# Optimization experiments

Measured on AMD Instinct MI355X. Metric: run time of the kernel, lower is better.

Reference implementation:

```python
import jax, jax.numpy as jnp
import numpy as np

# Dimensions: state [N, d, n, 2] with last axis = (q, p)
N, D, NN = 256, 8, 32
FEAT = D * NN          # flattened q features = 256
HID = 256              # MLP hidden width
DT = 0.01              # integration step
STEPS = 100            # number of RK4 steps (sequential)


def setup_inputs() -> dict:
    key = jax.random.key(0)
    k0, k1, k2 = jax.random.split(key, 3)
    x0 = 0.1 * jax.random.normal(k0, (N, D, NN, 2), dtype=jnp.float32)
    W1 = jax.random.normal(k1, (FEAT, HID), dtype=jnp.float32) / np.float32(np.sqrt(FEAT))
    b1 = jnp.zeros((HID,), dtype=jnp.float32)
    W2 = jax.random.normal(k2, (HID, 1), dtype=jnp.float32) / np.float32(np.sqrt(HID))
    b2 = jnp.zeros((1,), dtype=jnp.float32)
    return {"x0": x0, "W1": W1, "b1": b1, "W2": W2, "b2": b2}


def _hamiltonian(x, W1, b1, W2, b2):
    # x: [N, d, n, 2] -> H: [N]
    q = x[..., 0]
    p = x[..., 1]
    kinetic = 0.5 * jnp.sum(p * p, axis=(1, 2))          # [N]
    qf = q.reshape(q.shape[0], -1)                        # [N, d*n]
    h = jnp.tanh(qf @ W1 + b1)                            # [N, HID]
    V = (h @ W2 + b2)[:, 0]                               # [N]
    return kinetic + V


def _vector_field(x, params):
    # Hamiltonian vector field: dq/dt = dH/dp, dp/dt = -dH/dq (t-independent)
    g = jax.grad(lambda xx: jnp.sum(_hamiltonian(xx, *params)))(x)  # [N,d,n,2]
    return jnp.stack([g[..., 1], -g[..., 0]], axis=-1)


def _rk4_step(x, eps, params):
    k1 = _vector_field(x, params)
    k2 = _vector_field(x + 0.5 * eps * k1, params)
    k3 = _vector_field(x + 0.5 * eps * k2, params)
    k4 = _vector_field(x + eps * k3, params)
    return x + (eps / 6.0) * (k1 + 2.0 * k2 + 2.0 * k3 + k4)


def reference(x0, W1, b1, W2, b2):
    params = (W1, b1, W2, b2)
    eps = jnp.float32(DT)

    def step(x, _):
        return _rk4_step(x, eps, params), None

    xT, _ = jax.lax.scan(step, x0, None, length=STEPS)
    return xT
```

## Files before the change

kernel.cpp:

```cpp
#include <hip/hip_runtime.h>
#include <stdint.h>


typedef _Float16 v8h __attribute__((ext_vector_type(8)));
typedef float v4f __attribute__((ext_vector_type(4)));

#define NSTEPS 100
#define NEX 25
#define US 272

#define MFMA_AV(C, A, B) \
    asm("v_mfma_f32_16x16x32_f16 %0, %1, %2, %0" : "+v"(C) : "v"(A), "a"(B))

__device__ __forceinline__ float bfly4(float x) {
    float a = x, b = x;
    asm("v_permlane16_swap_b32 %0, %1" : "+v"(a), "+v"(b));
    float s = a + b;
    float c = s, d = s;
    asm("v_permlane32_swap_b32 %0, %1" : "+v"(c), "+v"(d));
    return c + d;
}

__device__ __forceinline__ float ueval2(float zz, float w4) {
    float e_ = __expf(zz);
    float r_ = __builtin_amdgcn_rcpf(e_ + 1.f);
    return w4 * __builtin_fmaf(-r_, r_, r_);
}

__global__ __launch_bounds__(256)
void ham_setup(const float* __restrict__ W1, _Float16* __restrict__ wt,
               _Float16* __restrict__ mf)
{
    const int b = blockIdx.x;
    const int t = threadIdx.x;
    wt[b * 256 + t] = (_Float16)W1[t * 256 + b];
    float acc = 0.f;
    #pragma unroll 4
    for (int r = 0; r < 256; ++r) {
        float wk = (float)(_Float16)W1[r * 256 + b];
        float wc = (float)(_Float16)W1[r * 256 + t];
        acc = __builtin_fmaf(wk, wc, acc);
    }
    mf[b * 256 + t] = (_Float16)acc;
}

__global__ __launch_bounds__(1024, 4)
void ham_kernel(const float* __restrict__ x0, const float* __restrict__ W1,
                const float* __restrict__ b1, const float* __restrict__ W2,
                const _Float16* __restrict__ wt, const _Float16* __restrict__ mf,
                float* __restrict__ out)
{
    __shared__ __align__(128) _Float16 ubuf[2 * 16 * US];

    const int t = threadIdx.x;
    const int w = t >> 6;
    const int l = t & 63;
    const int quad = l >> 4;
    const int s = l & 15;
    const int c0 = 16 * w + s;
    const int blk = blockIdx.x;
    const int kq = 8 * quad;
    const int sel = (s & 3) * US;

    v8h wF0[8], wM0[8];
    #pragma unroll
    for (int kk = 0; kk < 8; ++kk) {
        wF0[kk] = *(const v8h*)(wt + c0 * 256 + 32 * kk + kq);
        wM0[kk] = *(const v8h*)(mf + c0 * 256 + 32 * kk + kq);
    }

    const float b1r0 = b1[c0];
    const float w4 = 4.f * W2[c0];
    float2 qp0 = ((const float2*)(x0 + (size_t)blk * 512))[c0];
    const float q0o0 = qp0.x, p0o0 = qp0.y;

    if (quad == 0) {
        ubuf[c0] = (_Float16)q0o0;
        ubuf[US + c0] = (_Float16)p0o0;
        ubuf[2 * US + c0] = (_Float16)0.f;
        ubuf[3 * US + c0] = (_Float16)0.f;
    }
    __syncthreads();
    float z1, P;
    {
        const _Float16* ab = ubuf + sel + 8 * quad;
        v4f C0a = {0.f,0.f,0.f,0.f}, C0b = {0.f,0.f,0.f,0.f};
        #pragma unroll
        for (int kk = 0; kk < 8; kk += 2) {
            v8h a0 = *(const v8h*)(ab + 32 * kk);
            v8h a1 = *(const v8h*)(ab + 32 * (kk + 1));
            C0a = __builtin_amdgcn_mfma_f32_16x16x32_f16(a0, wF0[kk], C0a, 0, 0, 0);
            C0b = __builtin_amdgcn_mfma_f32_16x16x32_f16(a1, wF0[kk + 1], C0b, 0, 0, 0);
        }
        v4f C0s = C0a + C0b;
        z1 = C0s[0] + b1r0;  P = C0s[1];
    }
    __syncthreads();

    const float dt = 0.01f, hdt = 0.005f, dt6 = 0.01f / 6.f;
    const float dtdt6 = dt * dt6, hdt2 = hdt * hdt, dthdt = dt * hdt;
    const float fourdt = 4.f * dt;
    const float qf  = (float)quad;
    const float cPn   = -(qf * 0.25f * dt6);
    const float K2cz1 = 2.f * qf * dt;
    const float K2B   = qf * (4.f - qf) * dtdt6 * 0.25f;
    const float K2Vn  = -(qf * dtdt6 * 0.5f);
    const float K2hdt = 2.f * hdt;
    const float K2hdt2n = -2.f * hdt2;
    const float K2dt  = 2.f * dt;
    const float K2dthdtn = -2.f * dthdt;
    const float wB  = 3.f - qf;

    const int cw = c0 ^ (quad << 3);
    const int R0 = 4 * quad;
    const int wo0 = (R0 + 0) * US + cw;
    const int wo1 = (R0 + 1) * US + (cw ^ 32);
    const int wo2 = (R0 + 2) * US + cw;
    const int wo3 = (R0 + 3) * US + (cw ^ 32);
    const int sx = (s >> 2) & 3;
    const int rbase = s * US + 8 * (quad ^ sx);
    const int sodd = (s & 1) << 5;
    const _Float16* pe = ubuf + rbase + sodd;
    const _Float16* po = ubuf + rbase + 32 - sodd;

    float SBp = 0.f, SVp = 0.f;
    float Y1L = 0.f, Y2L = 0.f;
    float S1p = 0.f, S23p = 0.f;
    float cn = 99.f - qf;

    #pragma unroll 1
    for (int e = 0; e < NEX; ++e) {
        const int bo = (e & 1) * (16 * US);

        float Pp  = __builtin_fmaf(cPn, SBp, P);
        float zp2 = __builtin_fmaf(K2cz1, P, z1 + z1);
        zp2 = __builtin_fmaf(K2B, SBp, zp2);
        zp2 = __builtin_fmaf(K2Vn, SVp, zp2);
        float zb2 = __builtin_fmaf(K2hdt, Pp, zp2);
        float zc2 = __builtin_fmaf(K2hdt2n, Y1L, zb2);
        float zd2 = __builtin_fmaf(K2dt, Pp, zp2);
        zd2 = __builtin_fmaf(K2dthdtn, Y2L, zd2);

        float ua = ueval2(zp2, w4);
        float ub = ueval2(zb2, w4);
        float uc = ueval2(zc2, w4);
        float ud = ueval2(zd2, w4);

        ubuf[bo + wo0] = (_Float16)ua;
        ubuf[bo + wo1] = (_Float16)ub;
        ubuf[bo + wo2] = (_Float16)uc;
        ubuf[bo + wo3] = (_Float16)ud;
        __syncthreads();

        v4f C0s;
        {
            v4f C0a = {0.f,0.f,0.f,0.f}, C0b = {0.f,0.f,0.f,0.f};
            #pragma unroll
            for (int kk = 0; kk < 8; kk += 2) {
                v8h a0 = *(const v8h*)(pe + bo + 32 * kk);
                v8h a1 = *(const v8h*)(po + bo + 32 * kk);
                MFMA_AV(C0a, a0, wM0[kk]);
                MFMA_AV(C0b, a1, wM0[kk + 1]);
            }
            C0s = C0a + C0b;
        }

        float Y1 = C0s[0], Y2 = C0s[1], Y3 = C0s[2], Y4 = C0s[3];
        float tA = Y2 + Y3;
        float A  = Y1 + tA;
        float B  = A + tA + Y4;
        float V  = __builtin_fmaf(wB, B, A);
        float SB = bfly4(B);
        float SV = bfly4(V);

        z1 = __builtin_fmaf(fourdt, P, z1);
        z1 = __builtin_fmaf(-dtdt6, SV, z1);
        P  = __builtin_fmaf(-dt6, SB, P);

        SBp = SB;  SVp = SV;  Y1L = Y1;  Y2L = Y2;

        float tv = ub + uc;
        float sp = __builtin_fmaf(2.f, tv, ua + ud);
        float sq = ua + tv;
        S1p += sp;
        S23p = __builtin_fmaf(cn, sp, S23p) + sq;
        cn -= 4.f;
    }

    v8h wBt0[8];
    #pragma unroll
    for (int kk = 0; kk < 8; ++kk) {
        const float* wp = W1 + c0 * 256 + 32 * kk + kq;
        v4f lo = *(const v4f*)(wp);
        v4f hi = *(const v4f*)(wp + 4);
        v8h h;
        h[0] = (_Float16)lo[0]; h[1] = (_Float16)lo[1];
        h[2] = (_Float16)lo[2]; h[3] = (_Float16)lo[3];
        h[4] = (_Float16)hi[0]; h[5] = (_Float16)hi[1];
        h[6] = (_Float16)hi[2]; h[7] = (_Float16)hi[3];
        wBt0[kk] = h;
    }

    const float S1f  = bfly4(S1p);
    const float S23f = bfly4(S23p);
    __syncthreads();
    if (quad == 0) {
        ubuf[c0] = (_Float16)S1f;
        ubuf[US + c0] = (_Float16)S23f;
        ubuf[2 * US + c0] = (_Float16)0.f;
        ubuf[3 * US + c0] = (_Float16)0.f;
    }
    __syncthreads();
    float D10, D20;
    {
        const _Float16* ab = ubuf + sel + 8 * quad;
        v4f C0a = {0.f,0.f,0.f,0.f}, C0b = {0.f,0.f,0.f,0.f};
        #pragma unroll
        for (int kk = 0; kk < 8; kk += 2) {
            v8h a0 = *(const v8h*)(ab + 32 * kk);
            v8h a1 = *(const v8h*)(ab + 32 * (kk + 1));
            C0a = __builtin_amdgcn_mfma_f32_16x16x32_f16(a0, wBt0[kk], C0a, 0, 0, 0);
            C0b = __builtin_amdgcn_mfma_f32_16x16x32_f16(a1, wBt0[kk + 1], C0b, 0, 0, 0);
        }
        v4f C0s = C0a + C0b;
        D10 = C0s[0];  D20 = C0s[1];
    }
    const float dt6e = 0.01f / 6.f, dtdt6e = 0.01f * dt6e;
    float pT0 = p0o0 - dt6e * D10;
    float qT0 = q0o0 + 0.01f * (float)NSTEPS * p0o0 - dtdt6e * D20;

    if (quad == 0)
        ((float2*)(out + (size_t)blk * 512))[c0] = make_float2(qT0, pT0);
}

extern "C" void kernel_launch(void* const* d_in, const int* in_sizes, int n_in,
                              void* d_out, int out_size, void* d_ws, size_t ws_size,
                              hipStream_t stream) {
    const float* x0 = (const float*)d_in[0];
    const float* W1 = (const float*)d_in[1];
    const float* b1 = (const float*)d_in[2];
    const float* W2 = (const float*)d_in[3];
    float* out = (float*)d_out;
    _Float16* wt = (_Float16*)d_ws;
    _Float16* mf = wt + 256 * 256;
    hipLaunchKernelGGL(ham_setup, dim3(256), dim3(256), 0, stream, W1, wt, mf);
    hipLaunchKernelGGL(ham_kernel, dim3(256), dim3(1024), 0, stream,
                       x0, W1, b1, W2, wt, mf, out);
}
```

Measured before the change: 109.9 us.

## Shrink block to 4 waves, each thread handling four hidden columns

The main kernel now launches 256 threads per block instead of 1024. Each thread owns four hidden units, holding four sets of weight fragments in registers and issuing four MFMA chains per step. The shared buffer layout moves from padded rows to an XOR swizzle with vectorized 4-wide half stores. Block barriers become cheaper, and the setup kernel reuses a shared column of W1 instead of reloading it. The cost is more serial MFMA and transcendental work per wave, plus higher register pressure, which could lengthen the sequential per-step critical path.

```diff
diff --git a/kernel.cpp b/kernel.cpp
--- a/kernel.cpp
+++ b/kernel.cpp
@@ -3,11 +3,10 @@
 
 
 typedef _Float16 v8h __attribute__((ext_vector_type(8)));
+typedef _Float16 v4h __attribute__((ext_vector_type(4)));
 typedef float v4f __attribute__((ext_vector_type(4)));
 
-#define NSTEPS 100
 #define NEX 25
-#define US 272
 
 #define MFMA_AV(C, A, B) \
     asm("v_mfma_f32_16x16x32_f16 %0, %1, %2, %0" : "+v"(C) : "v"(A), "a"(B))
@@ -31,69 +30,92 @@
 void ham_setup(const float* __restrict__ W1, _Float16* __restrict__ wt,
                _Float16* __restrict__ mf)
 {
+    __shared__ float colb[256];
     const int b = blockIdx.x;
     const int t = threadIdx.x;
-    wt[b * 256 + t] = (_Float16)W1[t * 256 + b];
+    float wv = W1[t * 256 + b];
+    wt[b * 256 + t] = (_Float16)wv;
+    colb[t] = (float)(_Float16)wv;
+    __syncthreads();
     float acc = 0.f;
-    #pragma unroll 4
+    #pragma unroll 8
     for (int r = 0; r < 256; ++r) {
-        float wk = (float)(_Float16)W1[r * 256 + b];
         float wc = (float)(_Float16)W1[r * 256 + t];
-        acc = __builtin_fmaf(wk, wc, acc);
+        acc = __builtin_fmaf(colb[r], wc, acc);
     }
     mf[b * 256 + t] = (_Float16)acc;
 }
 
-__global__ __launch_bounds__(1024, 4)
+__global__ __launch_bounds__(256, 1)
 void ham_kernel(const float* __restrict__ x0, const float* __restrict__ W1,
                 const float* __restrict__ b1, const float* __restrict__ W2,
                 const _Float16* __restrict__ wt, const _Float16* __restrict__ mf,
                 float* __restrict__ out)
 {
-    __shared__ __align__(128) _Float16 ubuf[2 * 16 * US];
+    __shared__ __align__(128) _Float16 ubuf[2 * 16 * 256];
 
     const int t = threadIdx.x;
     const int w = t >> 6;
     const int l = t & 63;
     const int quad = l >> 4;
     const int s = l & 15;
-    const int c0 = 16 * w + s;
     const int blk = blockIdx.x;
     const int kq = 8 * quad;
-    const int sel = (s & 3) * US;
-
-    v8h wF0[8], wM0[8];
+    const int cb = 64 * w + 4 * s;
+    const int chb = cb >> 3;
+    const int clo = cb & 7;
+
+    v8h wM[4][8];
     #pragma unroll
-    for (int kk = 0; kk < 8; ++kk) {
-        wF0[kk] = *(const v8h*)(wt + c0 * 256 + 32 * kk + kq);
-        wM0[kk] = *(const v8h*)(mf + c0 * 256 + 32 * kk + kq);
-    }
-
-    const float b1r0 = b1[c0];
-    const float w4 = 4.f * W2[c0];
-    float2 qp0 = ((const float2*)(x0 + (size_t)blk * 512))[c0];
-    const float q0o0 = qp0.x, p0o0 = qp0.y;
+    for (int tt = 0; tt < 4; ++tt)
+        #pragma unroll
+        for (int kk = 0; kk < 8; ++kk)
+            wM[tt][kk] = *(const v8h*)(mf + (cb + tt) * 256 + 32 * kk + kq);
+
+    float b1r[4], w4v[4];
+    #pragma unroll
+    for (int tt = 0; tt < 4; ++tt) {
+        b1r[tt] = b1[cb + tt];
+        w4v[tt] = 4.f * W2[cb + tt];
+    }
+    v4f qp01 = *(const v4f*)(x0 + (size_t)blk * 512 + 2 * cb);
+    v4f qp23 = *(const v4f*)(x0 + (size_t)blk * 512 + 2 * cb + 4);
+    float q0v[4] = {qp01[0], qp01[2], qp23[0], qp23[2]};
+    float p0v[4] = {qp01[1], qp01[3], qp23[1], qp23[3]};
 
     if (quad == 0) {
-        ubuf[c0] = (_Float16)q0o0;
-        ubuf[US + c0] = (_Float16)p0o0;
-        ubuf[2 * US + c0] = (_Float16)0.f;
-        ubuf[3 * US + c0] = (_Float16)0.f;
-    }
-    __syncthreads();
-    float z1, P;
+        v4h r0 = {(_Float16)q0v[0], (_Float16)q0v[1],
+                  (_Float16)q0v[2], (_Float16)q0v[3]};
+        v4h r1 = {(_Float16)p0v[0], (_Float16)p0v[1],
+                  (_Float16)p0v[2], (_Float16)p0v[3]};
+        v4h rz = {(_Float16)0.f, (_Float16)0.f, (_Float16)0.f, (_Float16)0.f};
+        *(v4h*)(ubuf + 0 * 256 + 8 * (chb ^ 0) + clo) = r0;
+        *(v4h*)(ubuf + 1 * 256 + 8 * (chb ^ 1) + clo) = r1;
+        *(v4h*)(ubuf + 2 * 256 + 8 * (chb ^ 2) + clo) = rz;
+        *(v4h*)(ubuf + 3 * 256 + 8 * (chb ^ 3) + clo) = rz;
+    }
+    __syncthreads();
+    float z1[4], P[4];
     {
-        const _Float16* ab = ubuf + sel + 8 * quad;
-        v4f C0a = {0.f,0.f,0.f,0.f}, C0b = {0.f,0.f,0.f,0.f};
-        #pragma unroll
-        for (int kk = 0; kk < 8; kk += 2) {
-            v8h a0 = *(const v8h*)(ab + 32 * kk);
-            v8h a1 = *(const v8h*)(ab + 32 * (kk + 1));
-            C0a = __builtin_amdgcn_mfma_f32_16x16x32_f16(a0, wF0[kk], C0a, 0, 0, 0);
-            C0b = __builtin_amdgcn_mfma_f32_16x16x32_f16(a1, wF0[kk + 1], C0b, 0, 0, 0);
-        }
-        v4f C0s = C0a + C0b;
-        z1 = C0s[0] + b1r0;  P = C0s[1];
+        const _Float16* ab = ubuf + (s & 3) * 256 + 8 * (quad ^ (s & 3));
+        v8h a[8];
+        #pragma unroll
+        for (int kk = 0; kk < 8; ++kk)
+            a[kk] = *(const v8h*)(ab + 32 * kk);
+        #pragma unroll
+        for (int tt = 0; tt < 4; ++tt) {
+            v4f Ca = {0.f,0.f,0.f,0.f}, Cb = {0.f,0.f,0.f,0.f};
+            #pragma unroll
+            for (int kk = 0; kk < 8; kk += 2) {
+                v8h f0 = *(const v8h*)(wt + (cb + tt) * 256 + 32 * kk + kq);
+                v8h f1 = *(const v8h*)(wt + (cb + tt) * 256 + 32 * (kk + 1) + kq);
+                Ca = __builtin_amdgcn_mfma_f32_16x16x32_f16(a[kk], f0, Ca, 0, 0, 0);
+                Cb = __builtin_amdgcn_mfma_f32_16x16x32_f16(a[kk + 1], f1, Cb, 0, 0, 0);
+            }
+            v4f Cs = Ca + Cb;
+            z1[tt] = Cs[0] + b1r[tt];
+            P[tt]  = Cs[1];
+        }
     }
     __syncthreads();
 
@@ -111,126 +133,165 @@
     const float K2dthdtn = -2.f * dthdt;
     const float wB  = 3.f - qf;
 
-    const int cw = c0 ^ (quad << 3);
+    const int bsw = (s >> 2) & 1;
+    const int rdbase = s * 256 + 8 * (quad ^ (s & 3));
+    const _Float16* pe = ubuf + rdbase + 32 * bsw;
+    const _Float16* po = ubuf + rdbase + 32 * (1 - bsw);
     const int R0 = 4 * quad;
-    const int wo0 = (R0 + 0) * US + cw;
-    const int wo1 = (R0 + 1) * US + (cw ^ 32);
-    const int wo2 = (R0 + 2) * US + cw;
-    const int wo3 = (R0 + 3) * US + (cw ^ 32);
-    const int sx = (s >> 2) & 3;
-    const int rbase = s * US + 8 * (quad ^ sx);
-    const int sodd = (s & 1) << 5;
-    const _Float16* pe = ubuf + rbase + sodd;
-    const _Float16* po = ubuf + rbase + 32 - sodd;
-
-    float SBp = 0.f, SVp = 0.f;
-    float Y1L = 0.f, Y2L = 0.f;
-    float S1p = 0.f, S23p = 0.f;
+    const int wo0 = (R0 + 0) * 256 + 8 * (chb ^ ((R0 + 0) & 7)) + clo;
+    const int wo1 = (R0 + 1) * 256 + 8 * (chb ^ ((R0 + 1) & 7)) + clo;
+    const int wo2 = (R0 + 2) * 256 + 8 * (chb ^ ((R0 + 2) & 7)) + clo;
+    const int wo3 = (R0 + 3) * 256 + 8 * (chb ^ ((R0 + 3) & 7)) + clo;
+
+    float SBp[4] = {0.f,0.f,0.f,0.f}, SVp[4] = {0.f,0.f,0.f,0.f};
+    float Y1L[4] = {0.f,0.f,0.f,0.f}, Y2L[4] = {0.f,0.f,0.f,0.f};
+    float S1p[4] = {0.f,0.f,0.f,0.f}, S23p[4] = {0.f,0.f,0.f,0.f};
     float cn = 99.f - qf;
 
     #pragma unroll 1
     for (int e = 0; e < NEX; ++e) {
-        const int bo = (e & 1) * (16 * US);
-
-        float Pp  = __builtin_fmaf(cPn, SBp, P);
-        float zp2 = __builtin_fmaf(K2cz1, P, z1 + z1);
-        zp2 = __builtin_fmaf(K2B, SBp, zp2);
-        zp2 = __builtin_fmaf(K2Vn, SVp, zp2);
-        float zb2 = __builtin_fmaf(K2hdt, Pp, zp2);
-        float zc2 = __builtin_fmaf(K2hdt2n, Y1L, zb2);
-        float zd2 = __builtin_fmaf(K2dt, Pp, zp2);
-        zd2 = __builtin_fmaf(K2dthdtn, Y2L, zd2);
-
-        float ua = ueval2(zp2, w4);
-        float ub = ueval2(zb2, w4);
-        float uc = ueval2(zc2, w4);
-        float ud = ueval2(zd2, w4);
-
-        ubuf[bo + wo0] = (_Float16)ua;
-        ubuf[bo + wo1] = (_Float16)ub;
-        ubuf[bo + wo2] = (_Float16)uc;
-        ubuf[bo + wo3] = (_Float16)ud;
+        const int bo = (e & 1) * 4096;
+
+        float ua[4], ub[4], uc[4], ud[4];
+        #pragma unroll
+        for (int tt = 0; tt < 4; ++tt) {
+            float Pp  = __builtin_fmaf(cPn, SBp[tt], P[tt]);
+            float zp2 = __builtin_fmaf(K2cz1, P[tt], z1[tt] + z1[tt]);
+            zp2 = __builtin_fmaf(K2B, SBp[tt], zp2);
+            zp2 = __builtin_fmaf(K2Vn, SVp[tt], zp2);
+            float zb2 = __builtin_fmaf(K2hdt, Pp, zp2);
+            float zc2 = __builtin_fmaf(K2hdt2n, Y1L[tt], zb2);
+            float zd2 = __builtin_fmaf(K2dt, Pp, zp2);
+            zd2 = __builtin_fmaf(K2dthdtn, Y2L[tt], zd2);
+            ua[tt] = ueval2(zp2, w4v[tt]);
+            ub[tt] = ueval2(zb2, w4v[tt]);
+            uc[tt] = ueval2(zc2, w4v[tt]);
+            ud[tt] = ueval2(zd2, w4v[tt]);
+        }
+
+        {
+            v4h ra = {(_Float16)ua[0], (_Float16)ua[1], (_Float16)ua[2], (_Float16)ua[3]};
+            v4h rb = {(_Float16)ub[0], (_Float16)ub[1], (_Float16)ub[2], (_Float16)ub[3]};
+            v4h rc = {(_Float16)uc[0], (_Float16)uc[1], (_Float16)uc[2], (_Float16)uc[3]};
+            v4h rd = {(_Float16)ud[0], (_Float16)ud[1], (_Float16)ud[2], (_Float16)ud[3]};
+            *(v4h*)(ubuf + bo + wo0) = ra;
+            *(v4h*)(ubuf + bo + wo1) = rb;
+            *(v4h*)(ubuf + bo + wo2) = rc;
+            *(v4h*)(ubuf + bo + wo3) = rd;
+        }
         __syncthreads();
 
-        v4f C0s;
-        {
-            v4f C0a = {0.f,0.f,0.f,0.f}, C0b = {0.f,0.f,0.f,0.f};
+        v8h a0 = *(const v8h*)(pe + bo);
+        v8h a1 = *(const v8h*)(po + bo);
+        v8h a2 = *(const v8h*)(pe + bo + 64);
+        v8h a3 = *(const v8h*)(po + bo + 64);
+        v8h a4 = *(const v8h*)(pe + bo + 128);
+        v8h a5 = *(const v8h*)(po + bo + 128);
+        v8h a6 = *(const v8h*)(pe + bo + 192);
+        v8h a7 = *(const v8h*)(po + bo + 192);
+        v4f Ca[4], Cb[4];
+        #pragma unroll
+        for (int tt = 0; tt < 4; ++tt) {
+            Ca[tt] = (v4f){0.f,0.f,0.f,0.f};
+            Cb[tt] = (v4f){0.f,0.f,0.f,0.f};
+            MFMA_AV(Ca[tt], a0, wM[tt][0]);
+            MFMA_AV(Cb[tt], a1, wM[tt][1]);
+            MFMA_AV(Ca[tt], a2, wM[tt][2]);
+            MFMA_AV(Cb[tt], a3, wM[tt][3]);
+            MFMA_AV(Ca[tt], a4, wM[tt][4]);
+            MFMA_AV(Cb[tt], a5, wM[tt][5]);
+            MFMA_AV(Ca[tt], a6, wM[tt][6]);
+            MFMA_AV(Cb[tt], a7, wM[tt][7]);
+        }
+
+        #pragma unroll
+        for (int tt = 0; tt < 4; ++tt) {
+            float tv = ub[tt] + uc[tt];
+            float sp = __builtin_fmaf(2.f, tv, ua[tt] + ud[tt]);
+            float sq = ua[tt] + tv;
+            S1p[tt] += sp;
+            S23p[tt] = __builtin_fmaf(cn, sp, S23p[tt]) + sq;
+        }
+        cn -= 4.f;
+
+        #pragma unroll
+        for (int tt = 0; tt < 4; ++tt) {
+            v4f Cs = Ca[tt] + Cb[tt];
+            float Y1 = Cs[0], Y2 = Cs[1], Y3 = Cs[2], Y4 = Cs[3];
+            float tA = Y2 + Y3;
+            float A  = Y1 + tA;
+            float B  = A + tA + Y4;
+            float V  = __builtin_fmaf(wB, B, A);
+            float SB = bfly4(B);
+            float SV = bfly4(V);
+            z1[tt] = __builtin_fmaf(fourdt, P[tt], z1[tt]);
+            z1[tt] = __builtin_fmaf(-dtdt6, SV, z1[tt]);
+            P[tt]  = __builtin_fmaf(-dt6, SB, P[tt]);
+            SBp[tt] = SB;  SVp[tt] = SV;  Y1L[tt] = Y1;  Y2L[tt] = Y2;
+        }
+    }
+
+    float S1f[4], S23f[4];
+    #pragma unroll
+    for (int tt = 0; tt < 4; ++tt) {
+        S1f[tt]  = bfly4(S1p[tt]);
+        S23f[tt] = bfly4(S23p[tt]);
+    }
+    __syncthreads();
+    if (quad == 0) {
+        v4h r0 = {(_Float16)S1f[0], (_Float16)S1f[1],
+                  (_Float16)S1f[2], (_Float16)S1f[3]};
+        v4h r1 = {(_Float16)S23f[0], (_Float16)S23f[1],
+                  (_Float16)S23f[2], (_Float16)S23f[3]};
+        v4h rz = {(_Float16)0.f, (_Float16)0.f, (_Float16)0.f, (_Float16)0.f};
+        *(v4h*)(ubuf + 0 * 256 + 8 * (chb ^ 0) + clo) = r0;
+        *(v4h*)(ubuf + 1 * 256 + 8 * (chb ^ 1) + clo) = r1;
+        *(v4h*)(ubuf + 2 * 256 + 8 * (chb ^ 2) + clo) = rz;
+        *(v4h*)(ubuf + 3 * 256 + 8 * (chb ^ 3) + clo) = rz;
+    }
+    __syncthreads();
+    float D1[4], D2[4];
+    {
+        const _Float16* ab = ubuf + (s & 3) * 256 + 8 * (quad ^ (s & 3));
+        v8h a[8];
+        #pragma unroll
+        for (int kk = 0; kk < 8; ++kk)
+            a[kk] = *(const v8h*)(ab + 32 * kk);
+        #pragma unroll
+        for (int tt = 0; tt < 4; ++tt) {
+            v4f Ca = {0.f,0.f,0.f,0.f}, Cb = {0.f,0.f,0.f,0.f};
             #pragma unroll
-            for (int kk = 0; kk < 8; kk += 2) {
-                v8h a0 = *(const v8h*)(pe + bo + 32 * kk);
-                v8h a1 = *(const v8h*)(po + bo + 32 * kk);
-                MFMA_AV(C0a, a0, wM0[kk]);
-                MFMA_AV(C0b, a1, wM0[kk + 1]);
+            for (int kk = 0; kk < 8; ++kk) {
+                const float* wp = W1 + (cb + tt) * 256 + 32 * kk + kq;
+                v4f lo = *(const v4f*)(wp);
+                v4f hi = *(const v4f*)(wp + 4);
+                v8h h;
+                h[0] = (_Float16)lo[0]; h[1] = (_Float16)lo[1];
+                h[2] = (_Float16)lo[2]; h[3] = (_Float16)lo[3];
+                h[4] = (_Float16)hi[0]; h[5] = (_Float16)hi[1];
+                h[6] = (_Float16)hi[2]; h[7] = (_Float16)hi[3];
+                if (kk & 1)
+                    Cb = __builtin_amdgcn_mfma_f32_16x16x32_f16(a[kk], h, Cb, 0, 0, 0);
+                else
+                    Ca = __builtin_amdgcn_mfma_f32_16x16x32_f16(a[kk], h, Ca, 0, 0, 0);
             }
-            C0s = C0a + C0b;
-        }
-
-        float Y1 = C0s[0], Y2 = C0s[1], Y3 = C0s[2], Y4 = C0s[3];
-        float tA = Y2 + Y3;
-        float A  = Y1 + tA;
-        float B  = A + tA + Y4;
-        float V  = __builtin_fmaf(wB, B, A);
-        float SB = bfly4(B);
-        float SV = bfly4(V);
-
-        z1 = __builtin_fmaf(fourdt, P, z1);
-        z1 = __builtin_fmaf(-dtdt6, SV, z1);
-        P  = __builtin_fmaf(-dt6, SB, P);
-
-        SBp = SB;  SVp = SV;  Y1L = Y1;  Y2L = Y2;
-
-        float tv = ub + uc;
-        float sp = __builtin_fmaf(2.f, tv, ua + ud);
-        float sq = ua + tv;
-        S1p += sp;
-        S23p = __builtin_fmaf(cn, sp, S23p) + sq;
-        cn -= 4.f;
-    }
-
-    v8h wBt0[8];
-    #pragma unroll
-    for (int kk = 0; kk < 8; ++kk) {
-        const float* wp = W1 + c0 * 256 + 32 * kk + kq;
-        v4f lo = *(const v4f*)(wp);
-        v4f hi = *(const v4f*)(wp + 4);
-        v8h h;
-        h[0] = (_Float16)lo[0]; h[1] = (_Float16)lo[1];
-        h[2] = (_Float16)lo[2]; h[3] = (_Float16)lo[3];
-        h[4] = (_Float16)hi[0]; h[5] = (_Float16)hi[1];
-        h[6] = (_Float16)hi[2]; h[7] = (_Float16)hi[3];
-        wBt0[kk] = h;
-    }
-
-    const float S1f  = bfly4(S1p);
-    const float S23f = bfly4(S23p);
-    __syncthreads();
+            v4f Cs = Ca + Cb;
+            D1[tt] = Cs[0];  D2[tt] = Cs[1];
+        }
+    }
+    const float dt6e = 0.01f / 6.f, dtdt6e = 0.01f * dt6e;
     if (quad == 0) {
-        ubuf[c0] = (_Float16)S1f;
-        ubuf[US + c0] = (_Float16)S23f;
-        ubuf[2 * US + c0] = (_Float16)0.f;
-        ubuf[3 * US + c0] = (_Float16)0.f;
-    }
-    __syncthreads();
-    float D10, D20;
-    {
-        const _Float16* ab = ubuf + sel + 8 * quad;
-        v4f C0a = {0.f,0.f,0.f,0.f}, C0b = {0.f,0.f,0.f,0.f};
-        #pragma unroll
-        for (int kk = 0; kk < 8; kk += 2) {
-            v8h a0 = *(const v8h*)(ab + 32 * kk);
-            v8h a1 = *(const v8h*)(ab + 32 * (kk + 1));
-            C0a = __builtin_amdgcn_mfma_f32_16x16x32_f16(a0, wBt0[kk], C0a, 0, 0, 0);
-            C0b = __builtin_amdgcn_mfma_f32_16x16x32_f16(a1, wBt0[kk + 1], C0b, 0, 0, 0);
-        }
-        v4f C0s = C0a + C0b;
-        D10 = C0s[0];  D20 = C0s[1];
-    }
-    const float dt6e = 0.01f / 6.f, dtdt6e = 0.01f * dt6e;
-    float pT0 = p0o0 - dt6e * D10;
-    float qT0 = q0o0 + 0.01f * (float)NSTEPS * p0o0 - dtdt6e * D20;
-
-    if (quad == 0)
-        ((float2*)(out + (size_t)blk * 512))[c0] = make_float2(qT0, pT0);
+        float pT[4], qT[4];
+        #pragma unroll
+        for (int tt = 0; tt < 4; ++tt) {
+            pT[tt] = p0v[tt] - dt6e * D1[tt];
+            qT[tt] = q0v[tt] + 0.01f * 100.f * p0v[tt] - dtdt6e * D2[tt];
+        }
+        v4f o01 = {qT[0], pT[0], qT[1], pT[1]};
+        v4f o23 = {qT[2], pT[2], qT[3], pT[3]};
+        *(v4f*)(out + (size_t)blk * 512 + 2 * cb) = o01;
+        *(v4f*)(out + (size_t)blk * 512 + 2 * cb + 4) = o23;
+    }
 }
 
 extern "C" void kernel_launch(void* const* d_in, const int* in_sizes, int n_in,
@@ -244,6 +305,6 @@
     _Float16* wt = (_Float16*)d_ws;
     _Float16* mf = wt + 256 * 256;
     hipLaunchKernelGGL(ham_setup, dim3(256), dim3(256), 0, stream, W1, wt, mf);
-    hipLaunchKernelGGL(ham_kernel, dim3(256), dim3(1024), 0, stream,
+    hipLaunchKernelGGL(ham_kernel, dim3(256), dim3(256), 0, stream,
                        x0, W1, b1, W2, wt, mf, out);
 }
```

After: 107.3 us. 2.4% less time.
